# Optimization experiments

Measured on AMD Instinct MI355X. Metric: run time of the kernel, lower is better.

The kernel has to match this reference:

```python
import jax, jax.numpy as jnp
import numpy as np

EPS = 1e-6

def _to_patches(x, p):
    # [B,C,H,W] -> [(B*hp*wp), C, p, p], matching einops 'b c (h p1) (w p2) -> (b h w) c p1 p2'
    B, C, H, W = x.shape
    hp, wp = H // p, W // p
    y = x.reshape(B, C, hp, p, wp, p).transpose(0, 2, 4, 1, 3, 5)
    return y.reshape(B * hp * wp, C, p, p)

def _from_patches(y, B, hp, wp, p):
    # [(B*hp*wp), O, p, p] -> [B, O, H, W]
    O = y.shape[1]
    y = y.reshape(B, hp, wp, O, p, p).transpose(0, 3, 1, 4, 2, 5)
    return y.reshape(B, O, hp * p, wp * p)

def _expert_conv(x, v, w, b, p, pad):
    # x: [B,C,H,W]; v: [B,K,hp,wp]; w: [K,O,I,kh,kw]; b: [K,O]
    B, C, H, W = x.shape
    hp, wp = H // p, W // p
    y = _to_patches(x, p)                               # [N,C,p,p]
    vr = v.transpose(0, 2, 3, 1).reshape(-1, v.shape[1])  # [N,K]
    K, O, I, kh, kw = w.shape
    aw = jnp.einsum('nk,koihw->noihw', vr, w)            # per-patch aggregated kernels
    ab = vr @ b                                          # [N,O]
    if kh == 1 and kw == 1:
        out = jnp.einsum('ncpq,noc->nopq', y, aw[..., 0, 0])
    else:
        conv1 = lambda yi, wi: jax.lax.conv_general_dilated(
            yi[None], wi, window_strides=(1, 1), padding=[(pad, pad), (pad, pad)])[0]
        out = jax.vmap(conv1)(y, aw)
    out = out + ab[:, :, None, None]
    return _from_patches(out, B, hp, wp, p)

def _ln2d(x, g, be):
    # channel-wise LayerNorm (NAFNet LayerNorm2d)
    mu = jnp.mean(x, axis=1, keepdims=True)
    var = jnp.var(x, axis=1, keepdims=True)
    return g[None, :, None, None] * (x - mu) * jax.lax.rsqrt(var + EPS) + be[None, :, None, None]

def _sg(x):
    x1, x2 = jnp.split(x, 2, axis=1)
    return x1 * x2


def setup_inputs() -> dict:
    key = jax.random.key(0)
    ks = jax.random.split(key, 16)
    B, C, H, W, P, K = 2, 64, 384, 384, 64, 5
    dw = 2 * C
    s = lambda fan: (2.0 / fan) ** 0.5  # kaiming-ish scale
    inp = jax.random.normal(ks[0], (B, C, H, W), jnp.float32)
    v = jax.random.normal(ks[1], (B, K, H // P, W // P), jnp.float32)
    return {
        'inp': inp, 'v': v,
        'w1': jax.random.normal(ks[2], (K, dw, C, 1, 1), jnp.float32) * s(C),
        'b1': jnp.zeros((K, dw), jnp.float32),
        'w2': jax.random.normal(ks[3], (K, dw, dw, 3, 3), jnp.float32) * s(dw * 9),
        'b2': jnp.zeros((K, dw), jnp.float32),
        'w3': jax.random.normal(ks[4], (K, C, dw // 2, 1, 1), jnp.float32) * s(dw // 2),
        'b3': jnp.zeros((K, C), jnp.float32),
        'wsca': jax.random.normal(ks[5], (K, dw // 2, dw // 2, 1, 1), jnp.float32) * s(dw // 2),
        'bsca': jnp.zeros((K, dw // 2), jnp.float32),
        'w4': jax.random.normal(ks[6], (K, 2 * C, C, 1, 1), jnp.float32) * s(C),
        'b4': jnp.zeros((K, 2 * C), jnp.float32),
        'w5': jax.random.normal(ks[7], (K, C, C, 1, 1), jnp.float32) * s(C),
        'b5': jnp.zeros((K, C), jnp.float32),
        'n1w': jnp.ones((C,), jnp.float32),
        'n1b': jnp.zeros((C,), jnp.float32),
        'n2w': jnp.ones((C,), jnp.float32),
        'n2b': jnp.zeros((C,), jnp.float32),
        'beta': 0.1 * jax.random.normal(ks[8], (1, C, 1, 1), jnp.float32),
        'gamma': 0.1 * jax.random.normal(ks[9], (1, C, 1, 1), jnp.float32),
        'patch_size': P,
    }


def reference(inp, v, w1, b1, w2, b2, w3, b3, wsca, bsca, w4, b4, w5, b5,
              n1w, n1b, n2w, n2b, beta, gamma, patch_size):
    p = int(patch_size)
    x = _ln2d(inp, n1w, n1b)
    x = _expert_conv(x, v, w1, b1, p, 0)
    x = _expert_conv(x, v, w2, b2, p, 1)
    keep_x = _sg(x)
    x = jnp.mean(keep_x, axis=(2, 3), keepdims=True)      # AdaptiveAvgPool2d(1)
    x = x * _expert_conv(keep_x, v, wsca, bsca, p, 0)
    x = _expert_conv(x, v, w3, b3, p, 0)
    y = inp + x * beta
    x = _expert_conv(_ln2d(y, n2w, n2b), v, w4, b4, p, 0)
    x = _sg(x)
    x = _expert_conv(x, v, w5, b5, p, 0)
    return (y + x * gamma, v)
```

## Files before the change

### kernel.cpp

```cpp
#include <hip/hip_runtime.h>
#include <hip/hip_bf16.h>

typedef __hip_bfloat16 bf16;
typedef unsigned short u16t;
typedef unsigned int u32t;
typedef __attribute__((ext_vector_type(8))) short short8;
typedef __attribute__((ext_vector_type(4))) float f32x4;

#define HH 384
#define WW 384
#define HWH 147456
#define EPSV 1e-6f

__device__ __forceinline__ u32t pk2(float a, float b) {
  bf16 lo = __float2bfloat16(a), hi = __float2bfloat16(b);
  return ((u32t)(*(u16t*)&hi) << 16) | (u32t)(*(u16t*)&lo);
}

__global__ __launch_bounds__(256) void k_prep(
    const float* __restrict__ v,
    const float* __restrict__ w1, const float* __restrict__ b1,
    const float* __restrict__ w2, const float* __restrict__ b2,
    const float* __restrict__ w3, const float* __restrict__ b3,
    const float* __restrict__ wsca, const float* __restrict__ bsca,
    const float* __restrict__ w4, const float* __restrict__ b4,
    const float* __restrict__ w5, const float* __restrict__ b5,
    bf16* __restrict__ aw1b, bf16* __restrict__ a4b, bf16* __restrict__ ascab,
    bf16* __restrict__ a3b, bf16* __restrict__ a5b,
    float* __restrict__ ab1, float* __restrict__ ab2, float* __restrict__ ab4,
    float* __restrict__ abscaf, float* __restrict__ ab3, float* __restrict__ ab5,
    bf16* __restrict__ aw2) {
  int bid = blockIdx.x;
  int n = bid >> 3, sc = bid & 7;
  int b = n / 36, ph = (n % 36) / 6, pw = n % 6;
  float vr[5];
#pragma unroll
  for (int k = 0; k < 5; ++k) vr[k] = v[((b*5 + k)*6 + ph)*6 + pw];
  int t = threadIdx.x;
  for (int j = sc*1024 + t; j < sc*1024 + 1024; j += 256) {
    float s1 = 0.f, s4 = 0.f;
#pragma unroll
    for (int k = 0; k < 5; ++k) {
      s1 += vr[k] * w1[k*8192 + j];
      s4 += vr[k] * w4[k*8192 + j];
    }
    int oc = j >> 6, ic = j & 63;
    int idx = n*8192 + oc*64 + (((ic >> 3) ^ (oc & 7)) << 3) + (ic & 7);
    aw1b[idx] = __float2bfloat16(s1);
    a4b[idx]  = __float2bfloat16(s4);
  }
  for (int j = sc*512 + t; j < sc*512 + 512; j += 256) {
    float ss = 0.f, s3 = 0.f, s5 = 0.f;
#pragma unroll
    for (int k = 0; k < 5; ++k) {
      ss += vr[k] * wsca[k*4096 + j];
      s3 += vr[k] * w3[k*4096 + j];
      s5 += vr[k] * w5[k*4096 + j];
    }
    int oc = j >> 6, ic = j & 63;
    int idx = n*4096 + oc*64 + (((ic >> 3) ^ (oc & 7)) << 3) + (ic & 7);
    ascab[idx] = __float2bfloat16(ss);
    a3b[idx]   = __float2bfloat16(s3);
    a5b[idx]   = __float2bfloat16(s5);
  }
  if (sc == 0) {
    if (t < 128) {
      float s1 = 0.f, s2 = 0.f, s4 = 0.f;
#pragma unroll
      for (int k = 0; k < 5; ++k) {
        s1 += vr[k] * b1[k*128 + t];
        s2 += vr[k] * b2[k*128 + t];
        s4 += vr[k] * b4[k*128 + t];
      }
      ab1[n*128 + t] = s1; ab2[n*128 + t] = s2; ab4[n*128 + t] = s4;
    } else if (t < 192) {
      int c = t - 128;
      float ss = 0.f, s3 = 0.f, s5 = 0.f;
#pragma unroll
      for (int k = 0; k < 5; ++k) {
        ss += vr[k] * bsca[k*64 + c];
        s3 += vr[k] * b3[k*64 + c];
        s5 += vr[k] * b5[k*64 + c];
      }
      abscaf[n*64 + c] = ss; ab3[n*64 + c] = s3; ab5[n*64 + c] = s5;
    }
  }
  for (int j = sc*18432 + t; j < sc*18432 + 18432; j += 256) {
    float s = 0.f;
#pragma unroll
    for (int k = 0; k < 5; ++k) s += vr[k] * w2[(size_t)k*147456 + j];
    int oc = j / 1152;
    int rr = j - oc*1152;
    int ic = rr / 9;
    int tt = rr - ic*9;
    int half = ic >> 6;
    int sl = (ic >> 3) & 7;
    aw2[(size_t)n*147456 + ((size_t)((tt*2 + half)*128 + oc) << 6)
        + (((sl ^ (oc & 7)) << 3) | (ic & 7))] = __float2bfloat16(s);
  }
}

__global__ __launch_bounds__(256) void k_ln_conv1(
    const float* __restrict__ inp, const bf16* __restrict__ aw1b,
    const float* __restrict__ ab1, const float* __restrict__ n1w,
    const float* __restrict__ n1b, bf16* __restrict__ x1) {
  __shared__ alignas(16) float xl[4096];
  __shared__ alignas(16) u16t wA[8192];
  __shared__ alignas(16) u16t lnb[4096];
  __shared__ float bl[128];
  __shared__ float gl[64], bel[64];
  __shared__ float ps[4][64], ps2[4][64];
  int bid = blockIdx.x;
  int b = bid / 2304; int rem = bid % 2304; int h = rem / 6; int pw = rem % 6;
  int ph = h >> 6; int n = (b*6 + ph)*6 + pw; int w0 = pw*64;
  int t = threadIdx.x;
  for (int j = t; j < 1024; j += 256)
    ((uint4*)wA)[j] = ((const uint4*)(aw1b + (size_t)n*8192))[j];
  if (t < 128) bl[t] = ab1[n*128 + t];
  if (t < 64) { gl[t] = n1w[t]; bel[t] = n1b[t]; }
  const float* ip = inp + ((size_t)b*64*HH + h)*WW + w0;
  for (int j = t; j < 4096; j += 256) {
    int c = j >> 6, px = j & 63;
    xl[j] = ip[(size_t)c*HWH + px];
  }
  __syncthreads();
  int px = t & 63, part = t >> 6;
  {
    float s = 0.f, s2 = 0.f;
    for (int c = part*16; c < part*16 + 16; ++c) { float xv = xl[c*64 + px]; s += xv; s2 += xv*xv; }
    ps[part][px] = s; ps2[part][px] = s2;
  }
  __syncthreads();
  float mu = (ps[0][px] + ps[1][px] + ps[2][px] + ps[3][px]) * (1.f/64.f);
  float var = (ps2[0][px] + ps2[1][px] + ps2[2][px] + ps2[3][px]) * (1.f/64.f) - mu*mu;
  float rs = rsqrtf(fmaxf(var, 0.f) + EPSV);
  {
    float lv[16];
#pragma unroll
    for (int cc = 0; cc < 16; ++cc) {
      int c = part*16 + cc;
      lv[cc] = (xl[c*64 + px] - mu) * rs * gl[c] + bel[c];
    }
    *(uint4*)&lnb[px*64 + (((part*2) ^ (px&7)) << 3)] =
        make_uint4(pk2(lv[0],lv[1]), pk2(lv[2],lv[3]), pk2(lv[4],lv[5]), pk2(lv[6],lv[7]));
    *(uint4*)&lnb[px*64 + (((part*2+1) ^ (px&7)) << 3)] =
        make_uint4(pk2(lv[8],lv[9]), pk2(lv[10],lv[11]), pk2(lv[12],lv[13]), pk2(lv[14],lv[15]));
  }
  __syncthreads();
  int wv = t >> 6, l = t & 63, ln = l & 15, lk = l >> 4;
  f32x4 acc[2][4];
#pragma unroll
  for (int i = 0; i < 2; ++i)
#pragma unroll
    for (int g = 0; g < 4; ++g)
#pragma unroll
      for (int rg = 0; rg < 4; ++rg)
        acc[i][g][rg] = bl[(2*wv + i)*16 + lk*4 + rg];
#pragma unroll
  for (int ch = 0; ch < 2; ++ch) {
    int slx = ((ch*4 + lk) ^ (ln & 7)) << 3;
    short8 a0 = *(const short8*)&wA[((2*wv + 0)*16 + ln)*64 + slx];
    short8 a1 = *(const short8*)&wA[((2*wv + 1)*16 + ln)*64 + slx];
#pragma unroll
    for (int g = 0; g < 4; ++g) {
      short8 bv = *(const short8*)&lnb[(g*16 + ln)*64 + slx];
      acc[0][g] = __builtin_amdgcn_mfma_f32_16x16x32_bf16(a0, bv, acc[0][g], 0, 0, 0);
      acc[1][g] = __builtin_amdgcn_mfma_f32_16x16x32_bf16(a1, bv, acc[1][g], 0, 0, 0);
    }
  }
  u16t* stg = (u16t*)xl;
#pragma unroll
  for (int i = 0; i < 2; ++i)
#pragma unroll
    for (int g = 0; g < 4; ++g) {
      int pxd = g*16 + ln;
      int g8 = (2*wv + i)*4 + lk;
      int st = g8 ^ (pxd & 15);
      *(uint2*)&stg[pxd*128 + (st << 2)] =
          make_uint2(pk2(acc[i][g][0], acc[i][g][1]), pk2(acc[i][g][2], acc[i][g][3]));
    }
  __syncthreads();
  bf16* xp = x1 + (((size_t)b*HH + h)*WW + w0)*128;
  for (int j = t; j < 2048; j += 256) {
    int pxd = j >> 5, gs = j & 31;
    uint2 val = *(uint2*)&stg[pxd*128 + (gs << 2)];
    *(uint2*)(xp + (size_t)pxd*128 + ((gs ^ (pxd & 15)) << 2)) = val;
  }
}

__global__ __launch_bounds__(256) void k_conv2m(
    const bf16* __restrict__ x1, const bf16* __restrict__ aw2,
    const float* __restrict__ ab2, bf16* __restrict__ kx, float* __restrict__ pool) {
  __shared__ alignas(16) u16t xs[4*66*64];
  __shared__ alignas(16) u16t wsA[8192];
  __shared__ alignas(16) u16t wsB[8192];
  __shared__ float pool_l[64];
  __shared__ float bias_l[128];
  int bid = blockIdx.x;
  int n = bid >> 5, rp = bid & 31;
  int b = n / 36, ph = (n % 36) / 6, pw = n % 6;
  int r0 = rp * 2;
  int t = threadIdx.x;
  if (t < 64) pool_l[t] = 0.f;
  if (t < 128) bias_l[t] = ab2[n*128 + t];

  const bf16* xbase = x1 + ((((size_t)b*HH + ph*64)*WW + pw*64) << 7);
  const bf16* wbase = aw2 + (size_t)n*147456;
  int wv = t >> 6, l = t & 63;
  int ln = l & 15, lk = l >> 4;
  int rr = wv >> 1;
  int cb0 = (wv & 1) * 32;
  f32x4 acc[8][2];
#pragma unroll
  for (int f = 0; f < 8; ++f)
#pragma unroll
    for (int g = 0; g < 2; ++g) acc[f][g] = (f32x4){0.f, 0.f, 0.f, 0.f};

  for (int icc = 0; icc < 2; ++icc) {
    __syncthreads();
    for (int j = t; j < 2112; j += 256) {
      int s_st = j & 7;
      int rc = j >> 3;
      int c = rc % 66, r = rc / 66;
      int gr = r0 + r - 1, gc = c - 1;
      uint4 val = make_uint4(0u, 0u, 0u, 0u);
      if (gr >= 0 && gr < 64 && gc >= 0 && gc < 64) {
        int s_orig = s_st ^ (c & 7);
        val = *(const uint4*)(xbase + (((size_t)gr*WW + gc) << 7) + icc*64 + s_orig*8);
      }
      *(uint4*)&xs[j*8] = val;
    }
    {
      const uint4* wp = (const uint4*)(wbase + (size_t)icc*8192);
#pragma unroll
      for (int i = 0; i < 4; ++i) ((uint4*)wsA)[i*256 + t] = wp[i*256 + t];
    }
    __syncthreads();

    uint4 stgld[4];
    for (int pos = 0; pos < 9; ++pos) {
      const u16t* wcur = (pos & 1) ? wsB : wsA;
      u16t* wnx = (pos & 1) ? wsA : wsB;
      int dh = pos / 3, dw = pos - dh*3;
      if (pos < 8) {
        const uint4* wp = (const uint4*)(wbase + (size_t)((pos + 1)*2 + icc)*8192);
#pragma unroll
        for (int i = 0; i < 4; ++i) stgld[i] = wp[i*256 + t];
      }
#pragma unroll
      for (int ch = 0; ch < 2; ++ch) {
        short8 af[8];
#pragma unroll
        for (int f = 0; f < 8; ++f) {
          int oc = f*16 + ln;
          int slot = (ch*4 + lk) ^ (oc & 7);
          af[f] = *(const short8*)&wcur[oc*64 + slot*8];
        }
#pragma unroll
        for (int g = 0; g < 2; ++g) {
          int cl = cb0 + g*16 + ln + dw;
          int row = rr + dh;
          int slot = (ch*4 + lk) ^ (cl & 7);
          short8 bfv = *(const short8*)&xs[(row*66 + cl)*64 + slot*8];
#pragma unroll
          for (int f = 0; f < 8; ++f)
            acc[f][g] = __builtin_amdgcn_mfma_f32_16x16x32_bf16(af[f], bfv, acc[f][g], 0, 0, 0);
        }
      }
      if (pos < 8) {
#pragma unroll
        for (int i = 0; i < 4; ++i) *(uint4*)&wnx[(i*256 + t)*8] = stgld[i];
        __syncthreads();
      }
    }
  }

  __syncthreads();
  u16t* stg = xs;
  float psum[4][4];
#pragma unroll
  for (int f = 0; f < 4; ++f)
#pragma unroll
    for (int rg = 0; rg < 4; ++rg) psum[f][rg] = 0.f;
#pragma unroll
  for (int f = 0; f < 4; ++f) {
#pragma unroll
    for (int g = 0; g < 2; ++g) {
      f32x4 lo = acc[f][g], hi = acc[f + 4][g];
      int col = cb0 + g*16 + ln;
      float kv[4];
#pragma unroll
      for (int rg = 0; rg < 4; ++rg) {
        int q = f*16 + lk*4 + rg;
        kv[rg] = (lo[rg] + bias_l[q]) * (hi[rg] + bias_l[64 + q]);
        psum[f][rg] += kv[rg];
      }
      int gq = f*4 + lk;
      int st = gq ^ (col & 15);
      *(uint2*)&stg[rr*4096 + col*64 + (st << 2)] =
          make_uint2(pk2(kv[0], kv[1]), pk2(kv[2], kv[3]));
    }
  }
#pragma unroll
  for (int f = 0; f < 4; ++f)
#pragma unroll
    for (int rg = 0; rg < 4; ++rg) {
      float s = psum[f][rg];
      s += __shfl_xor(s, 1); s += __shfl_xor(s, 2);
      s += __shfl_xor(s, 4); s += __shfl_xor(s, 8);
      if (ln == 0) atomicAdd(&pool_l[f*16 + lk*4 + rg], s);
    }
  __syncthreads();
  for (int j = t; j < 2048; j += 256) {
    int rr2 = j >> 10, remj = j & 1023, col = remj >> 4, gs = remj & 15;
    uint2 val = *(uint2*)&stg[rr2*4096 + col*64 + (gs << 2)];
    int hh2 = ph*64 + r0 + rr2;
    int gcol = pw*64 + col;
    *(uint2*)(kx + ((((size_t)b*HH + hh2)*WW + gcol) << 6) + ((gs ^ (col & 15)) << 2)) = val;
  }
  if (t < 64) atomicAdd(&pool[b*64 + t], pool_l[t]);
}

__global__ __launch_bounds__(256) void k_post1(
    const bf16* __restrict__ kxg, const float* __restrict__ inp,
    const float* __restrict__ pool,
    const bf16* __restrict__ ascab, const float* __restrict__ abscaf,
    const bf16* __restrict__ a3b, const float* __restrict__ ab3,
    const float* __restrict__ beta, float* __restrict__ yws) {
  __shared__ alignas(16) u16t wS[4096];
  __shared__ alignas(16) u16t w3S[4096];
  __shared__ alignas(16) u16t B1[4096];
  __shared__ alignas(16) u16t B2[4096];
  __shared__ float bsl[64], b3l[64], pol[64], betal[64];
  int bid = blockIdx.x;
  int b = bid / 2304; int rem = bid % 2304; int h = rem / 6; int pw = rem % 6;
  int ph = h >> 6; int n = (b*6 + ph)*6 + pw; int w0 = pw*64;
  int t = threadIdx.x;
  for (int j = t; j < 512; j += 256) {
    ((uint4*)wS)[j]  = ((const uint4*)(ascab + (size_t)n*4096))[j];
    ((uint4*)w3S)[j] = ((const uint4*)(a3b + (size_t)n*4096))[j];
  }
  if (t < 64) {
    bsl[t] = abscaf[n*64 + t];
    b3l[t] = ab3[n*64 + t];
    pol[t] = pool[b*64 + t] * (1.0f/147456.0f);
    betal[t] = beta[t];
  }
  const bf16* kxp = kxg + (((size_t)b*HH + h)*WW + w0)*64;
  for (int j = t; j < 512; j += 256) {
    int px = j >> 3, sl = j & 7;
    *(uint4*)&B1[px*64 + ((sl ^ (px & 7)) << 3)] = *(const uint4*)(kxp + px*64 + sl*8);
  }
  __syncthreads();
  int wv = t >> 6, l = t & 63, ln = l & 15, lk = l >> 4;
  f32x4 acc[4];
#pragma unroll
  for (int g = 0; g < 4; ++g)
#pragma unroll
    for (int rg = 0; rg < 4; ++rg) acc[g][rg] = bsl[wv*16 + lk*4 + rg];
#pragma unroll
  for (int ch = 0; ch < 2; ++ch) {
    int slx = ((ch*4 + lk) ^ (ln & 7)) << 3;
    short8 a = *(const short8*)&wS[(wv*16 + ln)*64 + slx];
#pragma unroll
    for (int g = 0; g < 4; ++g) {
      short8 bv = *(const short8*)&B1[(g*16 + ln)*64 + slx];
      acc[g] = __builtin_amdgcn_mfma_f32_16x16x32_bf16(a, bv, acc[g], 0, 0, 0);
    }
  }
#pragma unroll
  for (int g = 0; g < 4; ++g) {
    int px = g*16 + ln;
    float v[4];
#pragma unroll
    for (int rg = 0; rg < 4; ++rg) v[rg] = acc[g][rg] * pol[wv*16 + lk*4 + rg];
    int base = px*64 + (((2*wv + (lk >> 1)) ^ (px & 7)) << 3) + (lk & 1)*4;
    *(uint2*)&B2[base] = make_uint2(pk2(v[0], v[1]), pk2(v[2], v[3]));
  }
  __syncthreads();
  f32x4 acc2[4];
#pragma unroll
  for (int g = 0; g < 4; ++g)
#pragma unroll
    for (int rg = 0; rg < 4; ++rg) acc2[g][rg] = b3l[wv*16 + lk*4 + rg];
#pragma unroll
  for (int ch = 0; ch < 2; ++ch) {
    int slx = ((ch*4 + lk) ^ (ln & 7)) << 3;
    short8 a = *(const short8*)&w3S[(wv*16 + ln)*64 + slx];
#pragma unroll
    for (int g = 0; g < 4; ++g) {
      short8 bv = *(const short8*)&B2[(g*16 + ln)*64 + slx];
      acc2[g] = __builtin_amdgcn_mfma_f32_16x16x32_bf16(a, bv, acc2[g], 0, 0, 0);
    }
  }
  const float* inpp = inp + ((size_t)b*64*HH + h)*WW + w0;
  float* yp = yws + ((size_t)b*64*HH + h)*WW + w0;
#pragma unroll
  for (int g = 0; g < 4; ++g) {
    int px = g*16 + ln;
#pragma unroll
    for (int rg = 0; rg < 4; ++rg) {
      int oc = wv*16 + lk*4 + rg;
      yp[(size_t)oc*HWH + px] = inpp[(size_t)oc*HWH + px] + acc2[g][rg]*betal[oc];
    }
  }
}

__global__ __launch_bounds__(256) void k_post2(
    const float* __restrict__ yws,
    const bf16* __restrict__ a4b, const float* __restrict__ ab4,
    const bf16* __restrict__ a5b, const float* __restrict__ ab5,
    const float* __restrict__ n2w, const float* __restrict__ n2b,
    const float* __restrict__ gamma, float* __restrict__ outp) {
  __shared__ alignas(16) float yb[4096];
  __shared__ alignas(16) u16t w4S[8192];
  __shared__ alignas(16) u16t w5S[4096];
  __shared__ alignas(16) u16t pxb[4096];
  __shared__ float ps[4][64], ps2[4][64];
  __shared__ float b4l[128], b5l[64], gl[64], bel[64], gml[64];
  int bid = blockIdx.x;
  int b = bid / 2304; int rem = bid % 2304; int h = rem / 6; int pw = rem % 6;
  int ph = h >> 6; int n = (b*6 + ph)*6 + pw; int w0 = pw*64;
  int t = threadIdx.x;
  for (int j = t; j < 1024; j += 256)
    ((uint4*)w4S)[j] = ((const uint4*)(a4b + (size_t)n*8192))[j];
  for (int j = t; j < 512; j += 256)
    ((uint4*)w5S)[j] = ((const uint4*)(a5b + (size_t)n*4096))[j];
  if (t < 128) b4l[t] = ab4[n*128 + t];
  if (t < 64) {
    b5l[t] = ab5[n*64 + t];
    gl[t]  = n2w[t];
    bel[t] = n2b[t];
    gml[t] = gamma[t];
  }
  const float* yp = yws + ((size_t)b*64*HH + h)*WW + w0;
  for (int j = t; j < 4096; j += 256) {
    int c = j >> 6, px = j & 63;
    yb[j] = yp[(size_t)c*HWH + px];
  }
  __syncthreads();
  int px = t & 63, part = t >> 6;
  {
    float s = 0.f, s2 = 0.f;
    for (int c = part*16; c < part*16 + 16; ++c) { float yv = yb[c*64 + px]; s += yv; s2 += yv*yv; }
    ps[part][px] = s; ps2[part][px] = s2;
  }
  __syncthreads();
  float mu = (ps[0][px] + ps[1][px] + ps[2][px] + ps[3][px]) * (1.f/64.f);
  float var = (ps2[0][px] + ps2[1][px] + ps2[2][px] + ps2[3][px]) * (1.f/64.f) - mu*mu;
  float rs = rsqrtf(fmaxf(var, 0.f) + EPSV);
  {
    float lv[16];
#pragma unroll
    for (int cc = 0; cc < 16; ++cc) {
      int c = part*16 + cc;
      lv[cc] = (yb[c*64 + px] - mu) * rs * gl[c] + bel[c];
    }
    *(uint4*)&pxb[px*64 + (((part*2) ^ (px&7)) << 3)] =
        make_uint4(pk2(lv[0],lv[1]), pk2(lv[2],lv[3]), pk2(lv[4],lv[5]), pk2(lv[6],lv[7]));
    *(uint4*)&pxb[px*64 + (((part*2+1) ^ (px&7)) << 3)] =
        make_uint4(pk2(lv[8],lv[9]), pk2(lv[10],lv[11]), pk2(lv[12],lv[13]), pk2(lv[14],lv[15]));
  }
  __syncthreads();
  int wv = t >> 6, l = t & 63, ln = l & 15, lk = l >> 4;
  f32x4 accL[4], accH[4];
#pragma unroll
  for (int g = 0; g < 4; ++g)
#pragma unroll
    for (int rg = 0; rg < 4; ++rg) {
      accL[g][rg] = b4l[wv*16 + lk*4 + rg];
      accH[g][rg] = b4l[64 + wv*16 + lk*4 + rg];
    }
#pragma unroll
  for (int ch = 0; ch < 2; ++ch) {
    int slx = ((ch*4 + lk) ^ (ln & 7)) << 3;
    short8 aLo = *(const short8*)&w4S[((wv)*16 + ln)*64 + slx];
    short8 aHi = *(const short8*)&w4S[((wv + 4)*16 + ln)*64 + slx];
#pragma unroll
    for (int g = 0; g < 4; ++g) {
      short8 bv = *(const short8*)&pxb[(g*16 + ln)*64 + slx];
      accL[g] = __builtin_amdgcn_mfma_f32_16x16x32_bf16(aLo, bv, accL[g], 0, 0, 0);
      accH[g] = __builtin_amdgcn_mfma_f32_16x16x32_bf16(aHi, bv, accH[g], 0, 0, 0);
    }
  }
  __syncthreads();
#pragma unroll
  for (int g = 0; g < 4; ++g) {
    int pxd = g*16 + ln;
    float v[4];
#pragma unroll
    for (int rg = 0; rg < 4; ++rg) v[rg] = accL[g][rg] * accH[g][rg];
    int base = pxd*64 + (((2*wv + (lk >> 1)) ^ (pxd & 7)) << 3) + (lk & 1)*4;
    *(uint2*)&pxb[base] = make_uint2(pk2(v[0], v[1]), pk2(v[2], v[3]));
  }
  __syncthreads();
  f32x4 acc2[4];
#pragma unroll
  for (int g = 0; g < 4; ++g)
#pragma unroll
    for (int rg = 0; rg < 4; ++rg) acc2[g][rg] = b5l[wv*16 + lk*4 + rg];
#pragma unroll
  for (int ch = 0; ch < 2; ++ch) {
    int slx = ((ch*4 + lk) ^ (ln & 7)) << 3;
    short8 a = *(const short8*)&w5S[(wv*16 + ln)*64 + slx];
#pragma unroll
    for (int g = 0; g < 4; ++g) {
      short8 bv = *(const short8*)&pxb[(g*16 + ln)*64 + slx];
      acc2[g] = __builtin_amdgcn_mfma_f32_16x16x32_bf16(a, bv, acc2[g], 0, 0, 0);
    }
  }
  float* op = outp + ((size_t)b*64*HH + h)*WW + w0;
#pragma unroll
  for (int g = 0; g < 4; ++g) {
    int pxd = g*16 + ln;
#pragma unroll
    for (int rg = 0; rg < 4; ++rg) {
      int oc = wv*16 + lk*4 + rg;
      op[(size_t)oc*HWH + pxd] = yb[oc*64 + pxd] + acc2[g][rg]*gml[oc];
    }
  }
}

extern "C" void kernel_launch(void* const* d_in, const int* in_sizes, int n_in,
                              void* d_out, int out_size, void* d_ws, size_t ws_size,
                              hipStream_t stream) {
  (void)in_sizes; (void)n_in; (void)out_size; (void)ws_size;
  const float* inp  = (const float*)d_in[0];
  const float* v    = (const float*)d_in[1];
  const float* w1   = (const float*)d_in[2];
  const float* b1   = (const float*)d_in[3];
  const float* w2   = (const float*)d_in[4];
  const float* b2   = (const float*)d_in[5];
  const float* w3   = (const float*)d_in[6];
  const float* b3   = (const float*)d_in[7];
  const float* wsca = (const float*)d_in[8];
  const float* bsca = (const float*)d_in[9];
  const float* w4   = (const float*)d_in[10];
  const float* b4   = (const float*)d_in[11];
  const float* w5   = (const float*)d_in[12];
  const float* b5   = (const float*)d_in[13];
  const float* n1w  = (const float*)d_in[14];
  const float* n1b  = (const float*)d_in[15];
  const float* n2w  = (const float*)d_in[16];
  const float* n2b  = (const float*)d_in[17];
  const float* beta = (const float*)d_in[18];
  const float* gamma= (const float*)d_in[19];

  float* wsf  = (float*)d_ws;
  float* pool = wsf;
  float* ab1  = wsf + 128;
  float* ab2  = ab1 + 9216;
  float* ab4  = ab2 + 9216;
  float* abscaf = ab4 + 9216;
  float* ab3  = abscaf + 4608;
  float* ab5  = ab3 + 4608;
  bf16* aw1b  = (bf16*)(ab5 + 4608);
  bf16* a4b   = aw1b + 589824;
  bf16* ascab = a4b + 589824;
  bf16* a3b   = ascab + 294912;
  bf16* a5b   = a3b + 294912;
  bf16* aw2   = a5b + 294912;
  bf16* x1    = aw2 + 10616832;
  bf16* kxb   = x1 + 37748736;
  float* out0 = (float*)d_out;
  float* yws  = out0;

  hipMemsetAsync(pool, 0, 128*sizeof(float), stream);
  k_prep<<<dim3(576), dim3(256), 0, stream>>>(v, w1, b1, w2, b2, w3, b3, wsca, bsca,
      w4, b4, w5, b5, aw1b, a4b, ascab, a3b, a5b, ab1, ab2, ab4, abscaf, ab3, ab5, aw2);
  k_ln_conv1<<<dim3(4608), dim3(256), 0, stream>>>(inp, aw1b, ab1, n1w, n1b, x1);
  k_conv2m<<<dim3(2304), dim3(256), 0, stream>>>(x1, aw2, ab2, kxb, pool);
  k_post1<<<dim3(4608), dim3(256), 0, stream>>>(kxb, inp, pool, ascab, abscaf, a3b, ab3, beta, yws);
  k_post2<<<dim3(4608), dim3(256), 0, stream>>>(yws, a4b, ab4, a5b, ab5, n2w, n2b, gamma, out0);
  hipMemcpyAsync((char*)d_out + (size_t)18874368*4, d_in[1], 360*4,
                 hipMemcpyDeviceToDevice, stream);
}
```

Baseline: 471.6 us.

## Fuse post1 and post2 kernels, keep y in registers for LayerNorm

```diff
diff --git a/kernel.cpp b/kernel.cpp
--- a/kernel.cpp
+++ b/kernel.cpp
@@ -321,17 +321,26 @@
   if (t < 64) atomicAdd(&pool[b*64 + t], pool_l[t]);
 }
 
-__global__ __launch_bounds__(256) void k_post1(
+__global__ __launch_bounds__(256) void k_post(
     const bf16* __restrict__ kxg, const float* __restrict__ inp,
     const float* __restrict__ pool,
     const bf16* __restrict__ ascab, const float* __restrict__ abscaf,
     const bf16* __restrict__ a3b, const float* __restrict__ ab3,
-    const float* __restrict__ beta, float* __restrict__ yws) {
+    const float* __restrict__ beta,
+    const bf16* __restrict__ a4b, const float* __restrict__ ab4,
+    const bf16* __restrict__ a5b, const float* __restrict__ ab5,
+    const float* __restrict__ n2w, const float* __restrict__ n2b,
+    const float* __restrict__ gamma, float* __restrict__ outp) {
   __shared__ alignas(16) u16t wS[4096];
   __shared__ alignas(16) u16t w3S[4096];
+  __shared__ alignas(16) u16t w4S[8192];
+  __shared__ alignas(16) u16t w5S[4096];
   __shared__ alignas(16) u16t B1[4096];
   __shared__ alignas(16) u16t B2[4096];
+  __shared__ alignas(16) u16t pxb[4096];
+  __shared__ float ps[4][64], ps2[4][64];
   __shared__ float bsl[64], b3l[64], pol[64], betal[64];
+  __shared__ float b4l[128], b5l[64], gl[64], bel[64], gml[64];
   int bid = blockIdx.x;
   int b = bid / 2304; int rem = bid % 2304; int h = rem / 6; int pw = rem % 6;
   int ph = h >> 6; int n = (b*6 + ph)*6 + pw; int w0 = pw*64;
@@ -339,12 +348,20 @@
   for (int j = t; j < 512; j += 256) {
     ((uint4*)wS)[j]  = ((const uint4*)(ascab + (size_t)n*4096))[j];
     ((uint4*)w3S)[j] = ((const uint4*)(a3b + (size_t)n*4096))[j];
-  }
+    ((uint4*)w5S)[j] = ((const uint4*)(a5b + (size_t)n*4096))[j];
+  }
+  for (int j = t; j < 1024; j += 256)
+    ((uint4*)w4S)[j] = ((const uint4*)(a4b + (size_t)n*8192))[j];
+  if (t < 128) b4l[t] = ab4[n*128 + t];
   if (t < 64) {
     bsl[t] = abscaf[n*64 + t];
     b3l[t] = ab3[n*64 + t];
     pol[t] = pool[b*64 + t] * (1.0f/147456.0f);
     betal[t] = beta[t];
+    b5l[t] = ab5[n*64 + t];
+    gl[t]  = n2w[t];
+    bel[t] = n2b[t];
+    gml[t] = gamma[t];
   }
   const bf16* kxp = kxg + (((size_t)b*HH + h)*WW + w0)*64;
   for (int j = t; j < 512; j += 256) {
@@ -371,11 +388,11 @@
 #pragma unroll
   for (int g = 0; g < 4; ++g) {
     int px = g*16 + ln;
-    float v[4];
-#pragma unroll
-    for (int rg = 0; rg < 4; ++rg) v[rg] = acc[g][rg] * pol[wv*16 + lk*4 + rg];
+    float vv[4];
+#pragma unroll
+    for (int rg = 0; rg < 4; ++rg) vv[rg] = acc[g][rg] * pol[wv*16 + lk*4 + rg];
     int base = px*64 + (((2*wv + (lk >> 1)) ^ (px & 7)) << 3) + (lk & 1)*4;
-    *(uint2*)&B2[base] = make_uint2(pk2(v[0], v[1]), pk2(v[2], v[3]));
+    *(uint2*)&B2[base] = make_uint2(pk2(vv[0], vv[1]), pk2(vv[2], vv[3]));
   }
   __syncthreads();
   f32x4 acc2[4];
@@ -394,75 +411,42 @@
     }
   }
   const float* inpp = inp + ((size_t)b*64*HH + h)*WW + w0;
-  float* yp = yws + ((size_t)b*64*HH + h)*WW + w0;
+  float yv[4][4];
 #pragma unroll
   for (int g = 0; g < 4; ++g) {
     int px = g*16 + ln;
 #pragma unroll
     for (int rg = 0; rg < 4; ++rg) {
       int oc = wv*16 + lk*4 + rg;
-      yp[(size_t)oc*HWH + px] = inpp[(size_t)oc*HWH + px] + acc2[g][rg]*betal[oc];
-    }
-  }
-}
-
-__global__ __launch_bounds__(256) void k_post2(
-    const float* __restrict__ yws,
-    const bf16* __restrict__ a4b, const float* __restrict__ ab4,
-    const bf16* __restrict__ a5b, const float* __restrict__ ab5,
-    const float* __restrict__ n2w, const float* __restrict__ n2b,
-    const float* __restrict__ gamma, float* __restrict__ outp) {
-  __shared__ alignas(16) float yb[4096];
-  __shared__ alignas(16) u16t w4S[8192];
-  __shared__ alignas(16) u16t w5S[4096];
-  __shared__ alignas(16) u16t pxb[4096];
-  __shared__ float ps[4][64], ps2[4][64];
-  __shared__ float b4l[128], b5l[64], gl[64], bel[64], gml[64];
-  int bid = blockIdx.x;
-  int b = bid / 2304; int rem = bid % 2304; int h = rem / 6; int pw = rem % 6;
-  int ph = h >> 6; int n = (b*6 + ph)*6 + pw; int w0 = pw*64;
-  int t = threadIdx.x;
-  for (int j = t; j < 1024; j += 256)
-    ((uint4*)w4S)[j] = ((const uint4*)(a4b + (size_t)n*8192))[j];
-  for (int j = t; j < 512; j += 256)
-    ((uint4*)w5S)[j] = ((const uint4*)(a5b + (size_t)n*4096))[j];
-  if (t < 128) b4l[t] = ab4[n*128 + t];
-  if (t < 64) {
-    b5l[t] = ab5[n*64 + t];
-    gl[t]  = n2w[t];
-    bel[t] = n2b[t];
-    gml[t] = gamma[t];
-  }
-  const float* yp = yws + ((size_t)b*64*HH + h)*WW + w0;
-  for (int j = t; j < 4096; j += 256) {
-    int c = j >> 6, px = j & 63;
-    yb[j] = yp[(size_t)c*HWH + px];
-  }
-  __syncthreads();
-  int px = t & 63, part = t >> 6;
-  {
-    float s = 0.f, s2 = 0.f;
-    for (int c = part*16; c < part*16 + 16; ++c) { float yv = yb[c*64 + px]; s += yv; s2 += yv*yv; }
-    ps[part][px] = s; ps2[part][px] = s2;
-  }
-  __syncthreads();
-  float mu = (ps[0][px] + ps[1][px] + ps[2][px] + ps[3][px]) * (1.f/64.f);
-  float var = (ps2[0][px] + ps2[1][px] + ps2[2][px] + ps2[3][px]) * (1.f/64.f) - mu*mu;
-  float rs = rsqrtf(fmaxf(var, 0.f) + EPSV);
-  {
-    float lv[16];
-#pragma unroll
-    for (int cc = 0; cc < 16; ++cc) {
-      int c = part*16 + cc;
-      lv[cc] = (yb[c*64 + px] - mu) * rs * gl[c] + bel[c];
-    }
-    *(uint4*)&pxb[px*64 + (((part*2) ^ (px&7)) << 3)] =
-        make_uint4(pk2(lv[0],lv[1]), pk2(lv[2],lv[3]), pk2(lv[4],lv[5]), pk2(lv[6],lv[7]));
-    *(uint4*)&pxb[px*64 + (((part*2+1) ^ (px&7)) << 3)] =
-        make_uint4(pk2(lv[8],lv[9]), pk2(lv[10],lv[11]), pk2(lv[12],lv[13]), pk2(lv[14],lv[15]));
-  }
-  __syncthreads();
-  int wv = t >> 6, l = t & 63, ln = l & 15, lk = l >> 4;
+      yv[g][rg] = inpp[(size_t)oc*HWH + px] + acc2[g][rg]*betal[oc];
+    }
+  }
+#pragma unroll
+  for (int g = 0; g < 4; ++g) {
+    float s = yv[g][0] + yv[g][1] + yv[g][2] + yv[g][3];
+    float s2 = yv[g][0]*yv[g][0] + yv[g][1]*yv[g][1]
+             + yv[g][2]*yv[g][2] + yv[g][3]*yv[g][3];
+    s += __shfl_xor(s, 16); s += __shfl_xor(s, 32);
+    s2 += __shfl_xor(s2, 16); s2 += __shfl_xor(s2, 32);
+    if (lk == 0) { ps[wv][g*16 + ln] = s; ps2[wv][g*16 + ln] = s2; }
+  }
+  __syncthreads();
+#pragma unroll
+  for (int g = 0; g < 4; ++g) {
+    int pxd = g*16 + ln;
+    float mu = (ps[0][pxd] + ps[1][pxd] + ps[2][pxd] + ps[3][pxd]) * (1.f/64.f);
+    float var = (ps2[0][pxd] + ps2[1][pxd] + ps2[2][pxd] + ps2[3][pxd]) * (1.f/64.f) - mu*mu;
+    float rs = rsqrtf(fmaxf(var, 0.f) + EPSV);
+    float lv[4];
+#pragma unroll
+    for (int rg = 0; rg < 4; ++rg) {
+      int oc = wv*16 + lk*4 + rg;
+      lv[rg] = (yv[g][rg] - mu) * rs * gl[oc] + bel[oc];
+    }
+    int base = pxd*64 + (((2*wv + (lk >> 1)) ^ (pxd & 7)) << 3) + (lk & 1)*4;
+    *(uint2*)&pxb[base] = make_uint2(pk2(lv[0], lv[1]), pk2(lv[2], lv[3]));
+  }
+  __syncthreads();
   f32x4 accL[4], accH[4];
 #pragma unroll
   for (int g = 0; g < 4; ++g)
@@ -487,18 +471,18 @@
 #pragma unroll
   for (int g = 0; g < 4; ++g) {
     int pxd = g*16 + ln;
-    float v[4];
-#pragma unroll
-    for (int rg = 0; rg < 4; ++rg) v[rg] = accL[g][rg] * accH[g][rg];
+    float vv[4];
+#pragma unroll
+    for (int rg = 0; rg < 4; ++rg) vv[rg] = accL[g][rg] * accH[g][rg];
     int base = pxd*64 + (((2*wv + (lk >> 1)) ^ (pxd & 7)) << 3) + (lk & 1)*4;
-    *(uint2*)&pxb[base] = make_uint2(pk2(v[0], v[1]), pk2(v[2], v[3]));
-  }
-  __syncthreads();
-  f32x4 acc2[4];
+    *(uint2*)&pxb[base] = make_uint2(pk2(vv[0], vv[1]), pk2(vv[2], vv[3]));
+  }
+  __syncthreads();
+  f32x4 acc5[4];
 #pragma unroll
   for (int g = 0; g < 4; ++g)
 #pragma unroll
-    for (int rg = 0; rg < 4; ++rg) acc2[g][rg] = b5l[wv*16 + lk*4 + rg];
+    for (int rg = 0; rg < 4; ++rg) acc5[g][rg] = b5l[wv*16 + lk*4 + rg];
 #pragma unroll
   for (int ch = 0; ch < 2; ++ch) {
     int slx = ((ch*4 + lk) ^ (ln & 7)) << 3;
@@ -506,7 +490,7 @@
 #pragma unroll
     for (int g = 0; g < 4; ++g) {
       short8 bv = *(const short8*)&pxb[(g*16 + ln)*64 + slx];
-      acc2[g] = __builtin_amdgcn_mfma_f32_16x16x32_bf16(a, bv, acc2[g], 0, 0, 0);
+      acc5[g] = __builtin_amdgcn_mfma_f32_16x16x32_bf16(a, bv, acc5[g], 0, 0, 0);
     }
   }
   float* op = outp + ((size_t)b*64*HH + h)*WW + w0;
@@ -516,7 +500,7 @@
 #pragma unroll
     for (int rg = 0; rg < 4; ++rg) {
       int oc = wv*16 + lk*4 + rg;
-      op[(size_t)oc*HWH + pxd] = yb[oc*64 + pxd] + acc2[g][rg]*gml[oc];
+      op[(size_t)oc*HWH + pxd] = yv[g][rg] + acc5[g][rg]*gml[oc];
     }
   }
 }
@@ -563,15 +547,14 @@
   bf16* x1    = aw2 + 10616832;
   bf16* kxb   = x1 + 37748736;
   float* out0 = (float*)d_out;
-  float* yws  = out0;
 
   hipMemsetAsync(pool, 0, 128*sizeof(float), stream);
   k_prep<<<dim3(576), dim3(256), 0, stream>>>(v, w1, b1, w2, b2, w3, b3, wsca, bsca,
       w4, b4, w5, b5, aw1b, a4b, ascab, a3b, a5b, ab1, ab2, ab4, abscaf, ab3, ab5, aw2);
   k_ln_conv1<<<dim3(4608), dim3(256), 0, stream>>>(inp, aw1b, ab1, n1w, n1b, x1);
   k_conv2m<<<dim3(2304), dim3(256), 0, stream>>>(x1, aw2, ab2, kxb, pool);
-  k_post1<<<dim3(4608), dim3(256), 0, stream>>>(kxb, inp, pool, ascab, abscaf, a3b, ab3, beta, yws);
-  k_post2<<<dim3(4608), dim3(256), 0, stream>>>(yws, a4b, ab4, a5b, ab5, n2w, n2b, gamma, out0);
+  k_post<<<dim3(4608), dim3(256), 0, stream>>>(kxb, inp, pool, ascab, abscaf, a3b, ab3,
+      beta, a4b, ab4, a5b, ab5, n2w, n2b, gamma, out0);
   hipMemcpyAsync((char*)d_out + (size_t)18874368*4, d_in[1], 360*4,
                  hipMemcpyDeviceToDevice, stream);
 }
```

New measurement: 442.9 us. -6.1%, faster.
